# Optimization experiments

Measured on AMD Instinct MI355X. Metric: run time of the kernel, lower is better.

The kernel has to match this reference:

```python
import jax, jax.numpy as jnp
import numpy as np

B, T, NM, DM, DI, DS, DR, DC, NC = 8, 512, 128, 512, 1024, 32, 32, 4, 100


def setup_inputs() -> dict:
    ks = jax.random.split(jax.random.key(0), 10)
    r = lambda i, shape, s: (jax.random.normal(ks[i], shape) * s).astype(jnp.float32)
    return {
        "x": jax.random.normal(ks[0], (B, T, NM), dtype=jnp.float32),
        "w_proj": r(1, (NM, DM), 0.05),
        "b_proj": jnp.zeros((DM,), jnp.float32),
        "rms_w": jnp.ones((DM,), jnp.float32),
        "w_in": r(2, (DM, 2 * DI), 0.02),
        "conv_w": r(3, (DI, 1, DC), 0.2),
        "conv_b": jnp.zeros((DI,), jnp.float32),
        "w_xproj": r(4, (DI, DR + 2 * DS), 0.02),
        "w_dt": r(5, (DR, DI), 0.1),
        "b_dt": jnp.full((DI,), -4.6, jnp.float32),  # softplus -> ~0.01 init dt
        "A_log": jnp.log(jnp.broadcast_to(jnp.arange(1, DS + 1, dtype=jnp.float32), (DI, DS))),
        "D": jnp.ones((DI,), jnp.float32),
        "w_out": r(6, (DI, DM), 0.02),
        "w_cls": r(7, (DM, NC), 0.05),
        "b_cls": jnp.zeros((NC,), jnp.float32),
    }


def _forward(x, w_proj, b_proj, rms_w, w_in, conv_w, conv_b, w_xproj, w_dt, b_dt,
             A_log, D, w_out, w_cls, b_cls):
    # LinearNorm input projection: (B,T,NM) -> (B,T,DM)
    h0 = x @ w_proj + b_proj
    # RMSNorm (pre-norm of the ResidualBlock)
    xn = h0 * jax.lax.rsqrt(jnp.mean(h0 * h0, axis=-1, keepdims=True) + 1e-5) * rms_w
    # MambaBlock: in_proj (no bias) -> split into ssm path and gate residual
    xr = xn @ w_in                       # (B,T,2*DI)
    xp, res = jnp.split(xr, 2, axis=-1)  # each (B,T,DI)
    # causal depthwise conv1d (torch pads d_conv-1 both sides then slices [:T])
    xc = jnp.transpose(xp, (0, 2, 1))    # (B,DI,T)
    xc = jax.lax.conv_general_dilated(
        xc, conv_w, window_strides=(1,), padding=((DC - 1, 0),),
        dimension_numbers=("NCH", "OIH", "NCH"), feature_group_count=DI)
    xc = xc + conv_b[None, :, None]
    xp = jax.nn.silu(jnp.transpose(xc, (0, 2, 1)))  # (B,T,DI)
    # input-dependent SSM parameters
    xdbl = xp @ w_xproj                              # (B,T,DR+2*DS)
    dt, Bm, Cm = jnp.split(xdbl, [DR, DR + DS], axis=-1)
    delta = jax.nn.softplus(dt @ w_dt + b_dt)        # (B,T,DI)
    A = -jnp.exp(A_log)                              # (DI,DS)

    # selective scan: h_t = exp(delta_t*A) h_{t-1} + (delta_t*u_t) B_t ; y_t = <h_t, C_t>
    def step(hprev, inp):
        d_t, B_t, C_t, u_t = inp                     # (B,DI),(B,DS),(B,DS),(B,DI)
        dA = jnp.exp(d_t[..., None] * A)             # (B,DI,DS)
        h = dA * hprev + (d_t * u_t)[..., None] * B_t[:, None, :]
        y = jnp.einsum("bds,bs->bd", h, C_t)
        return h, y

    xs = (jnp.swapaxes(delta, 0, 1), jnp.swapaxes(Bm, 0, 1),
          jnp.swapaxes(Cm, 0, 1), jnp.swapaxes(xp, 0, 1))
    h_init = jnp.zeros((B, DI, DS), dtype=x.dtype)
    _, ys = jax.lax.scan(step, h_init, xs)           # ys: (T,B,DI)
    y = jnp.swapaxes(ys, 0, 1) + xp * D              # skip term D*u
    y = y * jax.nn.silu(res)                         # gate
    enc = h0 + y @ w_out                             # residual add
    # NB: faithful to source: mean over dim=2 (feature dim) -> (B,T), T==DM
    pooled = jnp.mean(enc, axis=2)
    return pooled @ w_cls + b_cls                    # (B,NC)


def reference(x, w_proj, b_proj, rms_w, w_in, conv_w, conv_b, w_xproj, w_dt, b_dt,
              A_log, D, w_out, w_cls, b_cls):
    return _forward(x, w_proj, b_proj, rms_w, w_in, conv_w, conv_b, w_xproj,
                    w_dt, b_dt, A_log, D, w_out, w_cls, b_cls)
```

## Files before the change

kernel.cpp:

```cpp
#include <hip/hip_runtime.h>
#include <hip/hip_bf16.h>
#include <cstddef>

#define Bb 8
#define Tt 512
#define NM 128
#define DM 512
#define DI 1024
#define DS 32
#define DR 32
#define DC 4
#define NC 100
#define BT (Bb*Tt)
#define NCH 8
#define CL  64

typedef unsigned short ushort_t;
typedef unsigned int uint_t;
typedef __attribute__((ext_vector_type(8))) short bf8;
typedef __attribute__((ext_vector_type(4))) float f4;

__device__ __forceinline__ float softplus_f(float x) {
    return fmaxf(x, 0.f) + log1pf(expf(-fabsf(x)));
}
__device__ __forceinline__ float silu_fast(float x) {
    return __fdividef(x, 1.f + __expf(-x));
}
__device__ __forceinline__ ushort_t bf16_rne(float x) {
    uint_t u = __float_as_uint(x);
    uint_t r = u + 0x7FFFu + ((u >> 16) & 1u);
    return (ushort_t)(r >> 16);
}
__device__ __forceinline__ float bf16_tof(ushort_t h) {
    return __uint_as_float(((uint_t)h) << 16);
}
__device__ __forceinline__ uint_t packf(float v) {
    ushort_t h = bf16_rne(v);
    ushort_t l = bf16_rne(v - bf16_tof(h));
    return ((uint_t)h << 16) | (uint_t)l;
}
template<int CTRL>
__device__ __forceinline__ float qperm(float x) {
    return __int_as_float(__builtin_amdgcn_mov_dpp(__float_as_int(x), CTRL, 0xF, 0xF, true));
}
template<int PAT>
__device__ __forceinline__ float swz(float x) {
    return __int_as_float(__builtin_amdgcn_ds_swizzle(__float_as_int(x), PAT));
}

__global__ __launch_bounds__(256) void split_tr_kernel(
    const float* __restrict__ src, ushort_t* __restrict__ hi,
    ushort_t* __restrict__ lo, int K, int N,
    float4* __restrict__ zbase, int zcount)
{
    __shared__ ushort_t th[32][34], tl[32][34];
    const int k0 = blockIdx.y * 32, n0 = blockIdx.x * 32;
    if (zbase) {
        const int zi = (blockIdx.y * gridDim.x + blockIdx.x) * 256 + threadIdx.x;
        if (zi < zcount) zbase[zi] = make_float4(0.f, 0.f, 0.f, 0.f);
    }
    #pragma unroll
    for (int it = 0; it < 4; ++it) {
        const int idx = it * 256 + threadIdx.x;
        const int r = idx >> 5, c = idx & 31;
        const float v = src[(size_t)(k0 + r) * N + n0 + c];
        const ushort_t h = bf16_rne(v);
        th[c][r] = h;
        tl[c][r] = bf16_rne(v - bf16_tof(h));
    }
    __syncthreads();
    #pragma unroll
    for (int it = 0; it < 4; ++it) {
        const int idx = it * 256 + threadIdx.x;
        const int r = idx >> 5, c = idx & 31;
        hi[(size_t)(n0 + r) * K + k0 + c] = th[r][c];
        lo[(size_t)(n0 + r) * K + k0 + c] = tl[r][c];
    }
}

__global__ __launch_bounds__(512) void gemm_mfma_big(
    const uint_t* __restrict__ Apk, int lda,
    const ushort_t* __restrict__ Bhi,
    ushort_t* __restrict__ C, int N, int K)
{
    constexpr int BM = 128, BN = 128;
    constexpr int FM = 2, FN = 4;
    __shared__ ushort_t sA[BM][40];
    __shared__ ushort_t sB[BN][40];
    const int tid = threadIdx.x;
    const int wid = tid >> 6, l = tid & 63, l15 = l & 15, g = l >> 4;
    const int wm = (wid >> 1) * 32, wn = (wid & 1) * 64;
    const int bm0 = blockIdx.y * BM, bn0 = blockIdx.x * BN;

    f4 acc[FM][FN] = {};
    uint4 aR[2], bRh;

    auto loadG = [&](int k0) {
        #pragma unroll
        for (int r = 0; r < 2; ++r) {
            const int idx = r * 2048 + tid * 4;
            const int m = idx >> 5, k = idx & 31;
            aR[r] = *(const uint4*)(Apk + (size_t)(bm0 + m) * lda + k0 + k);
        }
        {
            const int idx = tid * 8;
            const int n = idx >> 5, k = idx & 31;
            bRh = *(const uint4*)(Bhi + (size_t)(bn0 + n) * K + k0 + k);
        }
    };
    auto stoL = [&]() {
        #pragma unroll
        for (int r = 0; r < 2; ++r) {
            const int idx = r * 2048 + tid * 4;
            const int m = idx >> 5, k = idx & 31;
            uint2 hh;
            hh.x = (aR[r].x >> 16) | (aR[r].y & 0xFFFF0000u);
            hh.y = (aR[r].z >> 16) | (aR[r].w & 0xFFFF0000u);
            *(uint2*)&sA[m][k] = hh;
        }
        {
            const int idx = tid * 8;
            const int n = idx >> 5, k = idx & 31;
            *(uint4*)&sB[n][k] = bRh;
        }
    };

    loadG(0);
    for (int k0 = 0; k0 < K; k0 += 32) {
        stoL();
        __syncthreads();
        if (k0 + 32 < K) loadG(k0 + 32);
        bf8 ah[FM], bh[FN];
        #pragma unroll
        for (int i = 0; i < FM; ++i)
            ah[i] = *(bf8*)&sA[wm + i * 16 + l15][g * 8];
        #pragma unroll
        for (int j = 0; j < FN; ++j)
            bh[j] = *(bf8*)&sB[wn + j * 16 + l15][g * 8];
        #pragma unroll
        for (int i = 0; i < FM; ++i)
            #pragma unroll
            for (int j = 0; j < FN; ++j)
                acc[i][j] = __builtin_amdgcn_mfma_f32_16x16x32_bf16(ah[i], bh[j], acc[i][j], 0, 0, 0);
        __syncthreads();
    }
    #pragma unroll
    for (int i = 0; i < FM; ++i)
        #pragma unroll
        for (int j = 0; j < FN; ++j)
            #pragma unroll
            for (int r = 0; r < 4; ++r) {
                const int m = bm0 + wm + i * 16 + g * 4 + r;
                const int n = bn0 + wn + j * 16 + l15;
                C[(size_t)m * N + n] = bf16_rne(acc[i][j][r]);
            }
}

__global__ __launch_bounds__(256) void gemm_mfma_x(
    const ushort_t* __restrict__ Abf,
    const ushort_t* __restrict__ Bhi,
    float* __restrict__ C, int K, int kseg)
{
    constexpr int BM = 64, BN = 96;
    constexpr int FM = 2, FN = 3;
    __shared__ ushort_t sAx[BM][40];
    __shared__ ushort_t sBx[BN][40];
    const int tid = threadIdx.x;
    const int wid = tid >> 6, l = tid & 63, l15 = l & 15, g = l >> 4;
    const int wm = (wid >> 1) * 32, wn = (wid & 1) * 48;
    const int bm0 = blockIdx.y * BM;
    const int kbeg = blockIdx.z * kseg;

    f4 acc[FM][FN] = {};
    uint4 aR;
    uint2 bRh[3];

    auto loadG = [&](int k0) {
        {
            const int idx = tid * 8;
            const int m = idx >> 5, k = idx & 31;
            aR = *(const uint4*)(Abf + (size_t)(bm0 + m) * K + k0 + k);
        }
        #pragma unroll
        for (int r = 0; r < 3; ++r) {
            const int idx = r * 1024 + tid * 4;
            const int n = idx >> 5, k = idx & 31;
            bRh[r] = *(const uint2*)(Bhi + (size_t)n * K + k0 + k);
        }
    };
    auto stoL = [&]() {
        {
            const int idx = tid * 8;
            const int m = idx >> 5, k = idx & 31;
            *(uint4*)&sAx[m][k] = aR;
        }
        #pragma unroll
        for (int r = 0; r < 3; ++r) {
            const int idx = r * 1024 + tid * 4;
            const int n = idx >> 5, k = idx & 31;
            *(uint2*)&sBx[n][k] = bRh[r];
        }
    };

    loadG(kbeg);
    for (int k0 = kbeg; k0 < kbeg + kseg; k0 += 32) {
        stoL();
        __syncthreads();
        if (k0 + 32 < kbeg + kseg) loadG(k0 + 32);
        bf8 ah[FM], bh[FN];
        #pragma unroll
        for (int i = 0; i < FM; ++i)
            ah[i] = *(bf8*)&sAx[wm + i * 16 + l15][g * 8];
        #pragma unroll
        for (int j = 0; j < FN; ++j)
            bh[j] = *(bf8*)&sBx[wn + j * 16 + l15][g * 8];
        #pragma unroll
        for (int i = 0; i < FM; ++i)
            #pragma unroll
            for (int j = 0; j < FN; ++j)
                acc[i][j] = __builtin_amdgcn_mfma_f32_16x16x32_bf16(ah[i], bh[j], acc[i][j], 0, 0, 0);
        __syncthreads();
    }
    #pragma unroll
    for (int i = 0; i < FM; ++i)
        #pragma unroll
        for (int j = 0; j < FN; ++j)
            #pragma unroll
            for (int r = 0; r < 4; ++r) {
                const int m = bm0 + wm + i * 16 + g * 4 + r;
                const int n = wn + j * 16 + l15;
                unsafeAtomicAdd(&C[(size_t)m * 96 + n], acc[i][j][r]);
            }
}

__global__ __launch_bounds__(256) void gemm_mfma_pool(
    const uint_t* __restrict__ Apk, int lda,
    const ushort_t* __restrict__ Bhi,
    float* __restrict__ pooled, float pscale,
    int N, int K, int kseg)
{
    constexpr int BM = 64, BN = 64;
    constexpr int FM = 2, FN = 2;
    __shared__ ushort_t sA[2][BM][40];
    __shared__ ushort_t sB[BN][40];
    const int tid = threadIdx.x;
    const int wid = tid >> 6, l = tid & 63, l15 = l & 15, g = l >> 4;
    const int wm = (wid >> 1) * 32, wn = (wid & 1) * 32;
    const int bm0 = blockIdx.y * BM, bn0 = blockIdx.x * BN;
    const int kbeg = blockIdx.z * kseg;

    f4 acc[FM][FN] = {};
    uint4 aR[2], bRh;

    auto loadG = [&](int k0) {
        #pragma unroll
        for (int r = 0; r < 2; ++r) {
            const int idx = r * 1024 + tid * 4;
            const int m = idx >> 5, k = idx & 31;
            aR[r] = *(const uint4*)(Apk + (size_t)(bm0 + m) * lda + k0 + k);
        }
        {
            const int idx = tid * 8;
            const int n = idx >> 5, k = idx & 31;
            bRh = *(const uint4*)(Bhi + (size_t)(bn0 + n) * K + k0 + k);
        }
    };
    auto stoL = [&]() {
        #pragma unroll
        for (int r = 0; r < 2; ++r) {
            const int idx = r * 1024 + tid * 4;
            const int m = idx >> 5, k = idx & 31;
            const uint_t u0 = aR[r].x, u1 = aR[r].y, u2 = aR[r].z, u3 = aR[r].w;
            uint2 hh, ll;
            hh.x = (u0 >> 16) | (u1 & 0xFFFF0000u);
            hh.y = (u2 >> 16) | (u3 & 0xFFFF0000u);
            ll.x = (u0 & 0xFFFFu) | (u1 << 16);
            ll.y = (u2 & 0xFFFFu) | (u3 << 16);
            *(uint2*)&sA[0][m][k] = hh;
            *(uint2*)&sA[1][m][k] = ll;
        }
        {
            const int idx = tid * 8;
            const int n = idx >> 5, k = idx & 31;
            *(uint4*)&sB[n][k] = bRh;
        }
    };

    loadG(kbeg);
    for (int k0 = kbeg; k0 < kbeg + kseg; k0 += 32) {
        stoL();
        __syncthreads();
        if (k0 + 32 < kbeg + kseg) loadG(k0 + 32);
        bf8 ah[FM], al_[FM], bh[FN];
        #pragma unroll
        for (int i = 0; i < FM; ++i) {
            ah[i]  = *(bf8*)&sA[0][wm + i * 16 + l15][g * 8];
            al_[i] = *(bf8*)&sA[1][wm + i * 16 + l15][g * 8];
        }
        #pragma unroll
        for (int j = 0; j < FN; ++j)
            bh[j] = *(bf8*)&sB[wn + j * 16 + l15][g * 8];
        #pragma unroll
        for (int i = 0; i < FM; ++i)
            #pragma unroll
            for (int j = 0; j < FN; ++j)
                acc[i][j] = __builtin_amdgcn_mfma_f32_16x16x32_bf16(ah[i], bh[j], acc[i][j], 0, 0, 0);
        #pragma unroll
        for (int i = 0; i < FM; ++i)
            #pragma unroll
            for (int j = 0; j < FN; ++j)
                acc[i][j] = __builtin_amdgcn_mfma_f32_16x16x32_bf16(al_[i], bh[j], acc[i][j], 0, 0, 0);
        __syncthreads();
    }
    #pragma unroll
    for (int i = 0; i < FM; ++i)
        #pragma unroll
        for (int r = 0; r < 4; ++r) {
            float sum = acc[i][0][r];
            #pragma unroll
            for (int j = 1; j < FN; ++j) sum += acc[i][j][r];
            sum += __shfl_xor(sum, 1);
            sum += __shfl_xor(sum, 2);
            sum += __shfl_xor(sum, 4);
            sum += __shfl_xor(sum, 8);
            if (l15 == 0)
                unsafeAtomicAdd(pooled + bm0 + wm + i * 16 + g * 4 + r, sum * pscale);
        }
}

template<int EPI, int TSTORE>
__global__ __launch_bounds__(256) void gemm64(
    const float* __restrict__ A, int lda,
    const float* __restrict__ B,
    const float* __restrict__ bias,
    float* __restrict__ C,
    int M, int N, int K)
{
    __shared__ float As[16][68];
    __shared__ float Bs[16][64];
    const int tid = threadIdx.x;
    const int bm = blockIdx.y * 64;
    const int bn = blockIdx.x * 64;
    const int tx = tid & 15;
    const int ty = tid >> 4;
    const int la_m = tid >> 2;
    const int la_k = (tid & 3) << 2;
    const int lb_k = tid >> 4;
    const int lb_n = (tid & 15) << 2;

    float acc[4][4] = {};
    for (int k0 = 0; k0 < K; k0 += 16) {
        float4 av = *(const float4*)(A + (size_t)(bm + la_m) * lda + k0 + la_k);
        As[la_k + 0][la_m] = av.x;
        As[la_k + 1][la_m] = av.y;
        As[la_k + 2][la_m] = av.z;
        As[la_k + 3][la_m] = av.w;
        const int gn = bn + lb_n;
        const float* bp = B + (size_t)(k0 + lb_k) * N + gn;
        float4 bv = *(const float4*)bp;
        *(float4*)&Bs[lb_k][lb_n] = bv;
        __syncthreads();
        #pragma unroll
        for (int k = 0; k < 16; ++k) {
            float4 a = *(const float4*)&As[k][ty << 2];
            float4 b = *(const float4*)&Bs[k][tx << 2];
            float ar[4] = {a.x, a.y, a.z, a.w};
            float br[4] = {b.x, b.y, b.z, b.w};
            #pragma unroll
            for (int i = 0; i < 4; ++i)
                #pragma unroll
                for (int j = 0; j < 4; ++j)
                    acc[i][j] = fmaf(ar[i], br[j], acc[i][j]);
        }
        __syncthreads();
    }
    if (TSTORE == 0) {
        #pragma unroll
        for (int i = 0; i < 4; ++i) {
            const int gm = bm + (ty << 2) + i;
            #pragma unroll
            for (int j = 0; j < 4; ++j) {
                const int gn = bn + (tx << 2) + j;
                float v = acc[i][j];
                if (EPI == 1) v += bias[gn];
                else if (EPI == 2) v = softplus_f(v + bias[gn]);
                C[(size_t)gm * N + gn] = v;
            }
        }
    } else {
        const int bq = bm >> 9;
        const int tt0 = (bm & (Tt - 1)) + (ty << 2);
        #pragma unroll
        for (int j = 0; j < 4; ++j) {
            const int gn = bn + (tx << 2) + j;
            float4 v;
            float* vv = (float*)&v;
            #pragma unroll
            for (int i = 0; i < 4; ++i) {
                float t = acc[i][j];
                if (EPI == 2) t = softplus_f(t + bias[gn]);
                vv[i] = t;
            }
            *(float4*)(C + ((size_t)bq * N + gn) * Tt + tt0) = v;
        }
    }
}

__global__ __launch_bounds__(256) void rms_kernel(
    const float* __restrict__ h0, const float* __restrict__ w,
    uint_t* __restrict__ xn_pk, float* __restrict__ pooled)
{
    const int row = blockIdx.x;
    const float* p = h0 + (size_t)row * DM;
    const int tid = threadIdx.x;
    float v0 = p[tid], v1 = p[tid + 256];
    float ss = v0 * v0 + v1 * v1;
    float sm = v0 + v1;
    #pragma unroll
    for (int m = 32; m; m >>= 1) {
        ss += __shfl_xor(ss, m);
        sm += __shfl_xor(sm, m);
    }
    __shared__ float wss[4], wsm[4];
    if ((tid & 63) == 0) { wss[tid >> 6] = ss; wsm[tid >> 6] = sm; }
    __syncthreads();
    const float tot = wss[0] + wss[1] + wss[2] + wss[3];
    if (tid == 0)
        unsafeAtomicAdd(pooled + row, (wsm[0] + wsm[1] + wsm[2] + wsm[3]) * (1.0f / DM));
    const float scale = rsqrtf(tot * (1.0f / DM) + 1e-5f);
    xn_pk[(size_t)row * DM + tid]       = packf(v0 * scale * w[tid]);
    xn_pk[(size_t)row * DM + tid + 256] = packf(v1 * scale * w[tid + 256]);
}

__global__ __launch_bounds__(256) void conv_tr_kernel(
    const ushort_t* __restrict__ xr, const float* __restrict__ cw,
    const float* __restrict__ cb, ushort_t* __restrict__ xp_bf,
    ushort_t* __restrict__ res_bf)
{
    __shared__ float tp[64][65];
    __shared__ float tr[64][65];
    const int di0 = blockIdx.x * 64;
    const int t0  = blockIdx.y * 64;
    const int b   = blockIdx.z;
    const int c  = threadIdx.x & 63;
    const int r4 = threadIdx.x >> 6;
    const int di = di0 + c;
    const float bias = cb[di];
    float w0 = cw[di * DC + 0], w1 = cw[di * DC + 1],
          w2 = cw[di * DC + 2], w3 = cw[di * DC + 3];
    #pragma unroll
    for (int rr = 0; rr < 64; rr += 4) {
        const int t = t0 + rr + r4;
        const int bt = b * Tt + t;
        float acc = bias;
        if (t >= 3) {
            acc = fmaf(w0, bf16_tof(xr[(size_t)(bt - 3) * (2 * DI) + di]), acc);
            acc = fmaf(w1, bf16_tof(xr[(size_t)(bt - 2) * (2 * DI) + di]), acc);
            acc = fmaf(w2, bf16_tof(xr[(size_t)(bt - 1) * (2 * DI) + di]), acc);
        } else {
            if (t >= 1) acc = fmaf(w2, bf16_tof(xr[(size_t)(bt - 1) * (2 * DI) + di]), acc);
            if (t >= 2) acc = fmaf(w1, bf16_tof(xr[(size_t)(bt - 2) * (2 * DI) + di]), acc);
        }
        acc = fmaf(w3, bf16_tof(xr[(size_t)bt * (2 * DI) + di]), acc);
        tp[rr + r4][c] = silu_fast(acc);
        tr[rr + r4][c] = bf16_tof(xr[(size_t)bt * (2 * DI) + DI + di]);
    }
    __syncthreads();
    #pragma unroll
    for (int dd = 0; dd < 64; dd += 4) {
        const int dw = dd + r4;
        const size_t o = ((size_t)b * DI + di0 + dw) * Tt + t0 + c;
        xp_bf[o]  = bf16_rne(tp[c][dw]);
        res_bf[o] = bf16_rne(tr[c][dw]);
    }
}

__global__ __launch_bounds__(256) void scan_fused(
    const float* __restrict__ deltaT, const float* __restrict__ xdbl,
    const ushort_t* __restrict__ xp_bf, const ushort_t* __restrict__ res_bf,
    const float* __restrict__ A_log, const float* __restrict__ Dvec,
    uint_t* __restrict__ y_pk)
{
    __shared__ uint_t   sBC[2][DS][68];
    __shared__ float    sD [2][8][68];
    __shared__ float    sDU[2][8][68];
    __shared__ ushort_t sU [2][8][68];
    __shared__ ushort_t sR [2][8][68];
    __shared__ float ylds[CL][9];
    const int tid = threadIdx.x;
    const int grp = tid >> 5;
    const int l5 = tid & 31;
    const int s = ((l5 & 1) << 4) | (l5 >> 1);
    const int b = blockIdx.x >> 7;
    const int di0 = (blockIdx.x & 127) << 3;
    const int sd_r = tid >> 5;
    const int sd_t = (tid & 31) << 1;
    const int bc_t = tid >> 2;
    const int bc_s = (tid & 3) << 3;

    float2 rd2;
    uint_t ru, rr_;
    float4 rB[2], rC[2];
    auto stage_regs = [&](int c) {
        const size_t rb = ((size_t)(b * DI + di0 + sd_r)) * Tt + c * CL + sd_t;
        rd2 = *(const float2*)(deltaT + rb);
        ru  = *(const uint_t*)(xp_bf + rb);
        rr_ = *(const uint_t*)(res_bf + rb);
        const float* src = xdbl + ((size_t)b * Tt + c * CL + bc_t) * 96;
        rB[0] = *(const float4*)(src + 32 + bc_s);
        rB[1] = *(const float4*)(src + 32 + bc_s + 4);
        rC[0] = *(const float4*)(src + 64 + bc_s);
        rC[1] = *(const float4*)(src + 64 + bc_s + 4);
    };
    auto write_lds = [&](int bb) {
        *(float2*)&sD[bb][sd_r][sd_t] = rd2;
        const float u0 = bf16_tof((ushort_t)(ru & 0xFFFFu));
        const float u1 = bf16_tof((ushort_t)(ru >> 16));
        float2 du2;
        du2.x = rd2.x * u0;
        du2.y = rd2.y * u1;
        *(float2*)&sDU[bb][sd_r][sd_t] = du2;
        *(uint_t*)&sU[bb][sd_r][sd_t] = ru;
        *(uint_t*)&sR[bb][sd_r][sd_t] = rr_;
        const float bv[8] = {rB[0].x, rB[0].y, rB[0].z, rB[0].w,
                             rB[1].x, rB[1].y, rB[1].z, rB[1].w};
        const float cv[8] = {rC[0].x, rC[0].y, rC[0].z, rC[0].w,
                             rC[1].x, rC[1].y, rC[1].z, rC[1].w};
        #pragma unroll
        for (int j = 0; j < 8; ++j)
            sBC[bb][bc_s + j][bc_t] =
                ((uint_t)bf16_rne(cv[j]) << 16) | (uint_t)bf16_rne(bv[j]);
    };

    const bool s4b = (l5 & 1) != 0;
    const bool s0b = (l5 & 2) != 0;
    const bool s1b = (l5 & 4) != 0;
    const bool s2b = (l5 & 8) != 0;
    const bool s3b = (l5 & 16) != 0;
    const int di = di0 + grp;
    const float Ads2 = -expf(A_log[di * DS + s]) * 1.44269504f;
    const float Dv = Dvec[di];
    float h = 0.f;

    stage_regs(0);
    write_lds(0);
    #pragma unroll 1
    for (int c = 0; c < NCH; ++c) {
        const int bb = c & 1;
        __syncthreads();
        if (c < NCH - 1) stage_regs(c + 1);
        #pragma unroll 1
        for (int t0 = 0; t0 < CL; t0 += 32) {
            float buf[16] = {};
            uint4 bc_c = *(const uint4*)&sBC[bb][s][t0];
            float4 dv_c = *(const float4*)&sD[bb][grp][t0];
            float4 du_c = *(const float4*)&sDU[bb][grp][t0];
            #pragma unroll
            for (int tq = 0; tq < 8; ++tq) {
                uint4 bc_n;
                float4 dv_n, du_n;
                if (tq < 7) {
                    const int tb = t0 + tq * 4 + 4;
                    bc_n = *(const uint4*)&sBC[bb][s][tb];
                    dv_n = *(const float4*)&sD[bb][grp][tb];
                    du_n = *(const float4*)&sDU[bb][grp][tb];
                }
                const uint_t bcv[4] = {bc_c.x, bc_c.y, bc_c.z, bc_c.w};
                const float dv[4] = {dv_c.x, dv_c.y, dv_c.z, dv_c.w};
                const float duv[4] = {du_c.x, du_c.y, du_c.z, du_c.w};
                #pragma unroll
                for (int q = 0; q < 4; ++q) {
                    const int tl = tq * 4 + q;
                    const float Bq = __uint_as_float(bcv[q] << 16);
                    const float Cq = __uint_as_float(bcv[q] & 0xFFFF0000u);
                    h = fmaf(__builtin_amdgcn_exp2f(dv[q] * Ads2), h, duv[q] * Bq);
                    const float ps = h * Cq;
                    const float pr = ps + qperm<0xB1>(ps);
                    const bool keep = ((tl & 16) != 0) == s4b;
                    buf[tl & 15] = keep ? pr : buf[tl & 15];
                }
                if (tq < 7) { bc_c = bc_n; dv_c = dv_n; du_c = du_n; }
            }
            #pragma unroll
            for (int i = 0; i < 16; ++i) buf[i] += qperm<0x4E>(buf[i]);
            float r8[8];
            #pragma unroll
            for (int i = 0; i < 8; ++i) r8[i] = s0b ? buf[2 * i + 1] : buf[2 * i];
            #pragma unroll
            for (int i = 0; i < 8; ++i) r8[i] += swz<0x101F>(r8[i]);
            float w4[4];
            #pragma unroll
            for (int i = 0; i < 4; ++i) w4[i] = s1b ? r8[2 * i + 1] : r8[2 * i];
            #pragma unroll
            for (int i = 0; i < 4; ++i) w4[i] += swz<0x201F>(w4[i]);
            float v2[2];
            v2[0] = s2b ? w4[1] : w4[0];
            v2[1] = s2b ? w4[3] : w4[2];
            v2[0] += swz<0x401F>(v2[0]);
            v2[1] += swz<0x401F>(v2[1]);
            const float yv = s3b ? v2[1] : v2[0];
            const float uself = bf16_tof(sU[bb][grp][t0 + s]);
            const float rself = bf16_tof(sR[bb][grp][t0 + s]);
            ylds[t0 + s][grp] = fmaf(uself, Dv, yv) * silu_fast(rself);
        }
        __syncthreads();
        {
            const int row = tid >> 2;
            const int q2 = (tid & 3) << 1;
            uint2 o;
            o.x = packf(ylds[row][q2 + 0]);
            o.y = packf(ylds[row][q2 + 1]);
            *(uint2*)(y_pk + ((size_t)b * Tt + c * CL + row) * DI + di0 + q2) = o;
        }
        if (c < NCH - 1) write_lds(bb ^ 1);
    }
}

__global__ __launch_bounds__(256) void cls_kernel(
    const float* __restrict__ pooled, const float* __restrict__ w_cls,
    const float* __restrict__ b_cls, float* __restrict__ out)
{
    const int idx = blockIdx.x * 256 + threadIdx.x;
    if (idx >= Bb * NC) return;
    const int b = idx / NC, c = idx % NC;
    float acc = b_cls[c];
    for (int t = 0; t < DM; ++t)
        acc = fmaf(pooled[b * DM + t], w_cls[t * NC + c], acc);
    out[idx] = acc;
}

extern "C" void kernel_launch(void* const* d_in, const int* in_sizes, int n_in,
                              void* d_out, int out_size, void* d_ws, size_t ws_size,
                              hipStream_t stream) {
    const float* x      = (const float*)d_in[0];
    const float* w_proj = (const float*)d_in[1];
    const float* b_proj = (const float*)d_in[2];
    const float* rms_w  = (const float*)d_in[3];
    const float* w_in   = (const float*)d_in[4];
    const float* conv_w = (const float*)d_in[5];
    const float* conv_b = (const float*)d_in[6];
    const float* w_xprj = (const float*)d_in[7];
    const float* w_dt   = (const float*)d_in[8];
    const float* b_dt   = (const float*)d_in[9];
    const float* A_log  = (const float*)d_in[10];
    const float* Dvec   = (const float*)d_in[11];
    const float* w_out  = (const float*)d_in[12];
    const float* w_cls  = (const float*)d_in[13];
    const float* b_cls  = (const float*)d_in[14];
    float* out = (float*)d_out;

    float* ws = (float*)d_ws;
    float* h0     = ws;
    float* xn     = h0 + (size_t)BT * DM;
    float* xr     = xn + (size_t)BT * DM;
    float* xpT    = xr + (size_t)BT * 2 * DI;
    float* resT   = xpT + (size_t)Bb * DI * Tt;
    float* xdbl   = resT + (size_t)Bb * DI * Tt;
    float* pooled = xdbl + (size_t)BT * 96;
    float* wsplit = pooled + 4096;
    float* deltaT = xr;
    uint_t* y_pk  = (uint_t*)(xr + (size_t)Bb * DI * Tt);
    uint_t* xn_pk = (uint_t*)xn;
    ushort_t* xr_bf  = (ushort_t*)xr;
    ushort_t* xp_bf  = (ushort_t*)xpT;
    ushort_t* res_bf = (ushort_t*)resT;

    ushort_t* w_in_hi  = (ushort_t*)wsplit;
    ushort_t* w_in_lo  = w_in_hi + (size_t)(2 * DI) * DM;
    ushort_t* w_out_hi = w_in_lo + (size_t)(2 * DI) * DM;
    ushort_t* w_out_lo = w_out_hi + (size_t)DM * DI;
    ushort_t* w_xp_hi  = w_out_lo + (size_t)DM * DI;
    ushort_t* w_xp_lo  = w_xp_hi + (size_t)96 * DI;

    split_tr_kernel<<<dim3(2 * DI / 32, DM / 32), 256, 0, stream>>>(
        w_in, w_in_hi, w_in_lo, DM, 2 * DI,
        (float4*)xdbl, (BT * 96 + 4096) / 4);
    split_tr_kernel<<<dim3(DM / 32, DI / 32), 256, 0, stream>>>(
        w_out, w_out_hi, w_out_lo, DI, DM, nullptr, 0);
    split_tr_kernel<<<dim3(96 / 32, DI / 32), 256, 0, stream>>>(
        w_xprj, w_xp_hi, w_xp_lo, DI, 96, nullptr, 0);
    gemm64<1,0><<<dim3(DM / 64, BT / 64), 256, 0, stream>>>(
        x, NM, w_proj, b_proj, h0, BT, DM, NM);
    rms_kernel<<<BT, 256, 0, stream>>>(h0, rms_w, xn_pk, pooled);
    gemm_mfma_big<<<dim3(2 * DI / 128, BT / 128), 512, 0, stream>>>(
        xn_pk, DM, w_in_hi, xr_bf, 2 * DI, DM);
    conv_tr_kernel<<<dim3(DI / 64, Tt / 64, Bb), 256, 0, stream>>>(
        xr_bf, conv_w, conv_b, xp_bf, res_bf);
    gemm_mfma_x<<<dim3(1, BT / 64, 8), 256, 0, stream>>>(
        xp_bf, w_xp_hi, xdbl, DI, DI / 8);
    gemm64<2,1><<<dim3(DI / 64, BT / 64), 256, 0, stream>>>(
        xdbl, 96, w_dt, b_dt, deltaT, BT, DI, DR);
    scan_fused<<<Bb * (DI / 8), 256, 0, stream>>>(
        deltaT, xdbl, xp_bf, res_bf, A_log, Dvec, y_pk);
    gemm_mfma_pool<<<dim3(DM / 64, BT / 64, 4), 256, 0, stream>>>(
        y_pk, DI, w_out_hi, pooled, 1.0f / DM, DM, DI, DI / 4);
    cls_kernel<<<(Bb * NC + 255) / 256, 256, 0, stream>>>(pooled, w_cls, b_cls, out);
}
```

Measured before the change: 242.5 us.

## Move input and dt projections to split-bf16 MFMA and merge prep kernels

Replaces the fp32 SIMT gemm64 for the input projection and the dt projection with MFMA kernels that use a three-term hi/lo bf16 split to keep near-fp32 accuracy. All the weight split/transpose launches, the x packing and the zeroing are merged into a single prep kernel, which removes several launches. The dt kernel converts xdbl to hi/lo in shared memory and applies softplus plus the transposed store in its epilogue. The cost is three MFMAs per tile where one would do, plus extra packing traffic for x.

```diff
diff --git a/kernel.cpp b/kernel.cpp
--- a/kernel.cpp
+++ b/kernel.cpp
@@ -48,17 +48,35 @@
     return __int_as_float(__builtin_amdgcn_ds_swizzle(__float_as_int(x), PAT));
 }
 
-__global__ __launch_bounds__(256) void split_tr_kernel(
-    const float* __restrict__ src, ushort_t* __restrict__ hi,
-    ushort_t* __restrict__ lo, int K, int N,
+__global__ __launch_bounds__(256) void prep_kernel(
+    const float* __restrict__ x, const float* __restrict__ w_in,
+    const float* __restrict__ w_out, const float* __restrict__ w_xp,
+    const float* __restrict__ w_pj, const float* __restrict__ w_dt,
+    uint_t* __restrict__ x_pk,
+    ushort_t* __restrict__ w_in_hi, ushort_t* __restrict__ w_in_lo,
+    ushort_t* __restrict__ w_out_hi, ushort_t* __restrict__ w_out_lo,
+    ushort_t* __restrict__ w_xp_hi, ushort_t* __restrict__ w_xp_lo,
+    ushort_t* __restrict__ w_pj_hi, ushort_t* __restrict__ w_pj_lo,
+    ushort_t* __restrict__ w_dt_hi, ushort_t* __restrict__ w_dt_lo,
     float4* __restrict__ zbase, int zcount)
 {
     __shared__ ushort_t th[32][34], tl[32][34];
-    const int k0 = blockIdx.y * 32, n0 = blockIdx.x * 32;
-    if (zbase) {
-        const int zi = (blockIdx.y * gridDim.x + blockIdx.x) * 256 + threadIdx.x;
-        if (zi < zcount) zbase[zi] = make_float4(0.f, 0.f, 0.f, 0.f);
-    }
+    const int bid = blockIdx.x;
+    const float* src;
+    ushort_t *hi, *lo;
+    int K, N, bx, by;
+    if (bid < 1024)      { src = w_in;  hi = w_in_hi;  lo = w_in_lo;  K = DM; N = 2 * DI; bx = bid & 63; by = bid >> 6; }
+    else if (bid < 1536) { const int i = bid - 1024; src = w_out; hi = w_out_hi; lo = w_out_lo; K = DI; N = DM; bx = i & 15; by = i >> 4; }
+    else if (bid < 1632) { const int i = bid - 1536; src = w_xp;  hi = w_xp_hi;  lo = w_xp_lo;  K = DI; N = 96; bx = i % 3; by = i / 3; }
+    else if (bid < 1696) { const int i = bid - 1632; src = w_pj;  hi = w_pj_hi;  lo = w_pj_lo;  K = NM; N = DM; bx = i & 15; by = i >> 4; }
+    else if (bid < 1728) { const int i = bid - 1696; src = w_dt;  hi = w_dt_hi;  lo = w_dt_lo;  K = DR; N = DI; bx = i; by = 0; }
+    else {
+        const int e = (bid - 1728) * 256 + threadIdx.x;
+        x_pk[e] = packf(x[e]);
+        if (e < zcount) zbase[e] = make_float4(0.f, 0.f, 0.f, 0.f);
+        return;
+    }
+    const int k0 = by * 32, n0 = bx * 32;
     #pragma unroll
     for (int it = 0; it < 4; ++it) {
         const int idx = it * 256 + threadIdx.x;
@@ -78,19 +96,184 @@
     }
 }
 
+__global__ __launch_bounds__(512) void gemm_mfma_h0(
+    const uint_t* __restrict__ Apk,
+    const ushort_t* __restrict__ Bhi, const ushort_t* __restrict__ Blo,
+    const float* __restrict__ bias, float* __restrict__ C)
+{
+    constexpr int BM = 128, BN = 128, FM = 2, FN = 4, K = NM, N = DM;
+    __shared__ ushort_t sA[2][BM][40];
+    __shared__ ushort_t sB[2][BN][40];
+    const int tid = threadIdx.x;
+    const int wid = tid >> 6, l = tid & 63, l15 = l & 15, g = l >> 4;
+    const int wm = (wid >> 1) * 32, wn = (wid & 1) * 64;
+    const int bm0 = blockIdx.y * BM, bn0 = blockIdx.x * BN;
+
+    f4 acc[FM][FN] = {};
+    uint4 aR[2], bRh, bRl;
+
+    auto loadG = [&](int k0) {
+        #pragma unroll
+        for (int r = 0; r < 2; ++r) {
+            const int idx = r * 2048 + tid * 4;
+            const int m = idx >> 5, k = idx & 31;
+            aR[r] = *(const uint4*)(Apk + (size_t)(bm0 + m) * K + k0 + k);
+        }
+        {
+            const int idx = tid * 8;
+            const int n = idx >> 5, k = idx & 31;
+            const size_t o = (size_t)(bn0 + n) * K + k0 + k;
+            bRh = *(const uint4*)(Bhi + o);
+            bRl = *(const uint4*)(Blo + o);
+        }
+    };
+    auto stoL = [&]() {
+        #pragma unroll
+        for (int r = 0; r < 2; ++r) {
+            const int idx = r * 2048 + tid * 4;
+            const int m = idx >> 5, k = idx & 31;
+            uint2 hh, ll;
+            hh.x = (aR[r].x >> 16) | (aR[r].y & 0xFFFF0000u);
+            hh.y = (aR[r].z >> 16) | (aR[r].w & 0xFFFF0000u);
+            ll.x = (aR[r].x & 0xFFFFu) | (aR[r].y << 16);
+            ll.y = (aR[r].z & 0xFFFFu) | (aR[r].w << 16);
+            *(uint2*)&sA[0][m][k] = hh;
+            *(uint2*)&sA[1][m][k] = ll;
+        }
+        {
+            const int idx = tid * 8;
+            const int n = idx >> 5, k = idx & 31;
+            *(uint4*)&sB[0][n][k] = bRh;
+            *(uint4*)&sB[1][n][k] = bRl;
+        }
+    };
+
+    loadG(0);
+    for (int k0 = 0; k0 < K; k0 += 32) {
+        stoL();
+        __syncthreads();
+        if (k0 + 32 < K) loadG(k0 + 32);
+        bf8 ah[FM], al_[FM], bh[FN], bl_[FN];
+        #pragma unroll
+        for (int i = 0; i < FM; ++i) {
+            ah[i]  = *(bf8*)&sA[0][wm + i * 16 + l15][g * 8];
+            al_[i] = *(bf8*)&sA[1][wm + i * 16 + l15][g * 8];
+        }
+        #pragma unroll
+        for (int j = 0; j < FN; ++j) {
+            bh[j]  = *(bf8*)&sB[0][wn + j * 16 + l15][g * 8];
+            bl_[j] = *(bf8*)&sB[1][wn + j * 16 + l15][g * 8];
+        }
+        #pragma unroll
+        for (int i = 0; i < FM; ++i)
+            #pragma unroll
+            for (int j = 0; j < FN; ++j)
+                acc[i][j] = __builtin_amdgcn_mfma_f32_16x16x32_bf16(ah[i], bh[j], acc[i][j], 0, 0, 0);
+        #pragma unroll
+        for (int i = 0; i < FM; ++i)
+            #pragma unroll
+            for (int j = 0; j < FN; ++j)
+                acc[i][j] = __builtin_amdgcn_mfma_f32_16x16x32_bf16(al_[i], bh[j], acc[i][j], 0, 0, 0);
+        #pragma unroll
+        for (int i = 0; i < FM; ++i)
+            #pragma unroll
+            for (int j = 0; j < FN; ++j)
+                acc[i][j] = __builtin_amdgcn_mfma_f32_16x16x32_bf16(ah[i], bl_[j], acc[i][j], 0, 0, 0);
+        __syncthreads();
+    }
+    #pragma unroll
+    for (int i = 0; i < FM; ++i)
+        #pragma unroll
+        for (int j = 0; j < FN; ++j)
+            #pragma unroll
+            for (int r = 0; r < 4; ++r) {
+                const int m = bm0 + wm + i * 16 + g * 4 + r;
+                const int n = bn0 + wn + j * 16 + l15;
+                C[(size_t)m * N + n] = acc[i][j][r] + bias[n];
+            }
+}
+
+__global__ __launch_bounds__(256) void gemm_mfma_dt(
+    const float* __restrict__ xdbl,
+    const ushort_t* __restrict__ Bhi, const ushort_t* __restrict__ Blo,
+    const float* __restrict__ bias, float* __restrict__ dT)
+{
+    constexpr int FM = 2, FN = 2;
+    __shared__ ushort_t sA[2][64][40];
+    __shared__ ushort_t sB[2][64][40];
+    const int tid = threadIdx.x;
+    const int wid = tid >> 6, l = tid & 63, l15 = l & 15, g = l >> 4;
+    const int wm = (wid >> 1) * 32, wn = (wid & 1) * 32;
+    const int bm0 = blockIdx.y * 64, bn0 = blockIdx.x * 64;
+
+    #pragma unroll
+    for (int r = 0; r < 2; ++r) {
+        const int idx = r * 1024 + tid * 4;
+        const int m = idx >> 5, k = idx & 31;
+        const float4 v = *(const float4*)(xdbl + (size_t)(bm0 + m) * 96 + k);
+        const float vv[4] = {v.x, v.y, v.z, v.w};
+        #pragma unroll
+        for (int q = 0; q < 4; ++q) {
+            const ushort_t h = bf16_rne(vv[q]);
+            sA[0][m][k + q] = h;
+            sA[1][m][k + q] = bf16_rne(vv[q] - bf16_tof(h));
+        }
+    }
+    {
+        const int idx = tid * 8;
+        const int n = idx >> 5, k = idx & 31;
+        *(uint4*)&sB[0][n][k] = *(const uint4*)(Bhi + (size_t)(bn0 + n) * 32 + k);
+        *(uint4*)&sB[1][n][k] = *(const uint4*)(Blo + (size_t)(bn0 + n) * 32 + k);
+    }
+    __syncthreads();
+    f4 acc[FM][FN] = {};
+    bf8 ah[FM], al_[FM], bh[FN], bl_[FN];
+    #pragma unroll
+    for (int i = 0; i < FM; ++i) {
+        ah[i]  = *(bf8*)&sA[0][wm + i * 16 + l15][g * 8];
+        al_[i] = *(bf8*)&sA[1][wm + i * 16 + l15][g * 8];
+    }
+    #pragma unroll
+    for (int j = 0; j < FN; ++j) {
+        bh[j]  = *(bf8*)&sB[0][wn + j * 16 + l15][g * 8];
+        bl_[j] = *(bf8*)&sB[1][wn + j * 16 + l15][g * 8];
+    }
+    #pragma unroll
+    for (int i = 0; i < FM; ++i)
+        #pragma unroll
+        for (int j = 0; j < FN; ++j) {
+            acc[i][j] = __builtin_amdgcn_mfma_f32_16x16x32_bf16(ah[i], bh[j], acc[i][j], 0, 0, 0);
+            acc[i][j] = __builtin_amdgcn_mfma_f32_16x16x32_bf16(al_[i], bh[j], acc[i][j], 0, 0, 0);
+            acc[i][j] = __builtin_amdgcn_mfma_f32_16x16x32_bf16(ah[i], bl_[j], acc[i][j], 0, 0, 0);
+        }
+    #pragma unroll
+    for (int i = 0; i < FM; ++i)
+        #pragma unroll
+        for (int j = 0; j < FN; ++j) {
+            const int n = bn0 + wn + j * 16 + l15;
+            const int m0 = bm0 + wm + i * 16 + g * 4;
+            const float bn = bias[n];
+            float4 o;
+            o.x = softplus_f(acc[i][j][0] + bn);
+            o.y = softplus_f(acc[i][j][1] + bn);
+            o.z = softplus_f(acc[i][j][2] + bn);
+            o.w = softplus_f(acc[i][j][3] + bn);
+            *(float4*)(dT + ((size_t)(m0 >> 9) * DI + n) * Tt + (m0 & 511)) = o;
+        }
+}
+
 __global__ __launch_bounds__(512) void gemm_mfma_big(
     const uint_t* __restrict__ Apk, int lda,
     const ushort_t* __restrict__ Bhi,
     ushort_t* __restrict__ C, int N, int K)
 {
-    constexpr int BM = 128, BN = 128;
     constexpr int FM = 2, FN = 4;
-    __shared__ ushort_t sA[BM][40];
-    __shared__ ushort_t sB[BN][40];
+    __shared__ ushort_t sA[128][40];
+    __shared__ ushort_t sB[128][40];
     const int tid = threadIdx.x;
     const int wid = tid >> 6, l = tid & 63, l15 = l & 15, g = l >> 4;
     const int wm = (wid >> 1) * 32, wn = (wid & 1) * 64;
-    const int bm0 = blockIdx.y * BM, bn0 = blockIdx.x * BN;
+    const int bm0 = blockIdx.y * 128, bn0 = blockIdx.x * 128;
 
     f4 acc[FM][FN] = {};
     uint4 aR[2], bRh;
@@ -161,14 +344,13 @@
     const ushort_t* __restrict__ Bhi,
     float* __restrict__ C, int K, int kseg)
 {
-    constexpr int BM = 64, BN = 96;
     constexpr int FM = 2, FN = 3;
-    __shared__ ushort_t sAx[BM][40];
-    __shared__ ushort_t sBx[BN][40];
+    __shared__ ushort_t sAx[64][40];
+    __shared__ ushort_t sBx[96][40];
     const int tid = threadIdx.x;
     const int wid = tid >> 6, l = tid & 63, l15 = l & 15, g = l >> 4;
     const int wm = (wid >> 1) * 32, wn = (wid & 1) * 48;
-    const int bm0 = blockIdx.y * BM;
+    const int bm0 = blockIdx.y * 64;
     const int kbeg = blockIdx.z * kseg;
 
     f4 acc[FM][FN] = {};
@@ -239,14 +421,13 @@
     float* __restrict__ pooled, float pscale,
     int N, int K, int kseg)
 {
-    constexpr int BM = 64, BN = 64;
     constexpr int FM = 2, FN = 2;
-    __shared__ ushort_t sA[2][BM][40];
-    __shared__ ushort_t sB[BN][40];
+    __shared__ ushort_t sA[2][64][40];
+    __shared__ ushort_t sB[64][40];
     const int tid = threadIdx.x;
     const int wid = tid >> 6, l = tid & 63, l15 = l & 15, g = l >> 4;
     const int wm = (wid >> 1) * 32, wn = (wid & 1) * 32;
-    const int bm0 = blockIdx.y * BM, bn0 = blockIdx.x * BN;
+    const int bm0 = blockIdx.y * 64, bn0 = blockIdx.x * 64;
     const int kbeg = blockIdx.z * kseg;
 
     f4 acc[FM][FN] = {};
@@ -326,84 +507,6 @@
             if (l15 == 0)
                 unsafeAtomicAdd(pooled + bm0 + wm + i * 16 + g * 4 + r, sum * pscale);
         }
-}
-
-template<int EPI, int TSTORE>
-__global__ __launch_bounds__(256) void gemm64(
-    const float* __restrict__ A, int lda,
-    const float* __restrict__ B,
-    const float* __restrict__ bias,
-    float* __restrict__ C,
-    int M, int N, int K)
-{
-    __shared__ float As[16][68];
-    __shared__ float Bs[16][64];
-    const int tid = threadIdx.x;
-    const int bm = blockIdx.y * 64;
-    const int bn = blockIdx.x * 64;
-    const int tx = tid & 15;
-    const int ty = tid >> 4;
-    const int la_m = tid >> 2;
-    const int la_k = (tid & 3) << 2;
-    const int lb_k = tid >> 4;
-    const int lb_n = (tid & 15) << 2;
-
-    float acc[4][4] = {};
-    for (int k0 = 0; k0 < K; k0 += 16) {
-        float4 av = *(const float4*)(A + (size_t)(bm + la_m) * lda + k0 + la_k);
-        As[la_k + 0][la_m] = av.x;
-        As[la_k + 1][la_m] = av.y;
-        As[la_k + 2][la_m] = av.z;
-        As[la_k + 3][la_m] = av.w;
-        const int gn = bn + lb_n;
-        const float* bp = B + (size_t)(k0 + lb_k) * N + gn;
-        float4 bv = *(const float4*)bp;
-        *(float4*)&Bs[lb_k][lb_n] = bv;
-        __syncthreads();
-        #pragma unroll
-        for (int k = 0; k < 16; ++k) {
-            float4 a = *(const float4*)&As[k][ty << 2];
-            float4 b = *(const float4*)&Bs[k][tx << 2];
-            float ar[4] = {a.x, a.y, a.z, a.w};
-            float br[4] = {b.x, b.y, b.z, b.w};
-            #pragma unroll
-            for (int i = 0; i < 4; ++i)
-                #pragma unroll
-                for (int j = 0; j < 4; ++j)
-                    acc[i][j] = fmaf(ar[i], br[j], acc[i][j]);
-        }
-        __syncthreads();
-    }
-    if (TSTORE == 0) {
-        #pragma unroll
-        for (int i = 0; i < 4; ++i) {
-            const int gm = bm + (ty << 2) + i;
-            #pragma unroll
-            for (int j = 0; j < 4; ++j) {
-                const int gn = bn + (tx << 2) + j;
-                float v = acc[i][j];
-                if (EPI == 1) v += bias[gn];
-                else if (EPI == 2) v = softplus_f(v + bias[gn]);
-                C[(size_t)gm * N + gn] = v;
-            }
-        }
-    } else {
-        const int bq = bm >> 9;
-        const int tt0 = (bm & (Tt - 1)) + (ty << 2);
-        #pragma unroll
-        for (int j = 0; j < 4; ++j) {
-            const int gn = bn + (tx << 2) + j;
-            float4 v;
-            float* vv = (float*)&v;
-            #pragma unroll
-            for (int i = 0; i < 4; ++i) {
-                float t = acc[i][j];
-                if (EPI == 2) t = softplus_f(t + bias[gn]);
-                vv[i] = t;
-            }
-            *(float4*)(C + ((size_t)bq * N + gn) * Tt + tt0) = v;
-        }
-    }
 }
 
 __global__ __launch_bounds__(256) void rms_kernel(
@@ -671,16 +774,19 @@
     ushort_t* w_out_lo = w_out_hi + (size_t)DM * DI;
     ushort_t* w_xp_hi  = w_out_lo + (size_t)DM * DI;
     ushort_t* w_xp_lo  = w_xp_hi + (size_t)96 * DI;
-
-    split_tr_kernel<<<dim3(2 * DI / 32, DM / 32), 256, 0, stream>>>(
-        w_in, w_in_hi, w_in_lo, DM, 2 * DI,
+    ushort_t* w_pj_hi  = w_xp_lo + (size_t)96 * DI;
+    ushort_t* w_pj_lo  = w_pj_hi + (size_t)DM * NM;
+    ushort_t* w_dt_hi  = w_pj_lo + (size_t)DM * NM;
+    ushort_t* w_dt_lo  = w_dt_hi + (size_t)DI * DR;
+    uint_t*   x_pk     = (uint_t*)(w_dt_lo + (size_t)DI * DR);
+
+    prep_kernel<<<3776, 256, 0, stream>>>(
+        x, w_in, w_out, w_xprj, w_proj, w_dt, x_pk,
+        w_in_hi, w_in_lo, w_out_hi, w_out_lo, w_xp_hi, w_xp_lo,
+        w_pj_hi, w_pj_lo, w_dt_hi, w_dt_lo,
         (float4*)xdbl, (BT * 96 + 4096) / 4);
-    split_tr_kernel<<<dim3(DM / 32, DI / 32), 256, 0, stream>>>(
-        w_out, w_out_hi, w_out_lo, DI, DM, nullptr, 0);
-    split_tr_kernel<<<dim3(96 / 32, DI / 32), 256, 0, stream>>>(
-        w_xprj, w_xp_hi, w_xp_lo, DI, 96, nullptr, 0);
-    gemm64<1,0><<<dim3(DM / 64, BT / 64), 256, 0, stream>>>(
-        x, NM, w_proj, b_proj, h0, BT, DM, NM);
+    gemm_mfma_h0<<<dim3(DM / 128, BT / 128), 512, 0, stream>>>(
+        x_pk, w_pj_hi, w_pj_lo, b_proj, h0);
     rms_kernel<<<BT, 256, 0, stream>>>(h0, rms_w, xn_pk, pooled);
     gemm_mfma_big<<<dim3(2 * DI / 128, BT / 128), 512, 0, stream>>>(
         xn_pk, DM, w_in_hi, xr_bf, 2 * DI, DM);
@@ -688,8 +794,8 @@
         xr_bf, conv_w, conv_b, xp_bf, res_bf);
     gemm_mfma_x<<<dim3(1, BT / 64, 8), 256, 0, stream>>>(
         xp_bf, w_xp_hi, xdbl, DI, DI / 8);
-    gemm64<2,1><<<dim3(DI / 64, BT / 64), 256, 0, stream>>>(
-        xdbl, 96, w_dt, b_dt, deltaT, BT, DI, DR);
+    gemm_mfma_dt<<<dim3(DI / 64, BT / 64), 256, 0, stream>>>(
+        xdbl, w_dt_hi, w_dt_lo, b_dt, deltaT);
     scan_fused<<<Bb * (DI / 8), 256, 0, stream>>>(
         deltaT, xdbl, xp_bf, res_bf, A_log, Dvec, y_pk);
     gemm_mfma_pool<<<dim3(DM / 64, BT / 64, 4), 256, 0, stream>>>(
```

Result: faster. 231.3 us (-4.6%).
